# Optimization experiments

Hardware: AMD Instinct MI355X
Metric: run time of the kernel (lower is better)

Reference implementation:

```python
import jax, jax.numpy as jnp
import numpy as np

D_MODEL = 1024
N_HEADS = 16
HEAD_DIM = D_MODEL // N_HEADS


def setup_inputs() -> dict:
    key = jax.random.key(0)
    ks = jax.random.split(key, 5)
    B, S = 4, 2048
    scale = 1.0 / np.sqrt(D_MODEL)
    return {
        "x": jax.random.normal(ks[0], (B, S, D_MODEL), dtype=jnp.float32),
        "W_q": jax.random.normal(ks[1], (D_MODEL, D_MODEL), dtype=jnp.float32) * scale,
        "W_k": jax.random.normal(ks[2], (D_MODEL, D_MODEL), dtype=jnp.float32) * scale,
        "W_v": jax.random.normal(ks[3], (D_MODEL, D_MODEL), dtype=jnp.float32) * scale,
        "W_o": jax.random.normal(ks[4], (D_MODEL, D_MODEL), dtype=jnp.float32) * scale,
    }


def reference(x, W_q, W_k, W_v, W_o):
    B, S, _ = x.shape
    # nn.Linear(d,d,bias=False): y = x @ W.T ; W stored as (out,in)
    def proj(W):
        y = jnp.einsum('bsd,ed->bse', x, W)
        return y.reshape(B, S, N_HEADS, HEAD_DIM).transpose(0, 2, 1, 3)  # (B,H,S,Dh)
    q, k, v = proj(W_q), proj(W_k), proj(W_v)
    scores = jnp.einsum('bhqd,bhkd->bhqk', q, k) / np.sqrt(HEAD_DIM)
    causal = jnp.tril(jnp.ones((S, S), dtype=bool))  # (S,S)
    scores = jnp.where(causal[None, None], scores, -jnp.inf)
    attn = jax.nn.softmax(scores, axis=-1)
    heads = jnp.einsum('bhqk,bhkd->bhqd', attn, v)
    concat = heads.transpose(0, 2, 1, 3).reshape(B, S, D_MODEL)
    return jnp.einsum('bsd,ed->bse', concat, W_o)
```

## Files before the change

### kernel.cpp

```cpp
#include <hip/hip_runtime.h>
#include <hip/hip_bf16.h>

#define D_MODEL 1024
#define N_HEADS 16
#define HEAD_DIM 64
#define BATCH 4
#define SEQ 2048
#define M_ROWS (BATCH * SEQ)

typedef __attribute__((ext_vector_type(8))) __bf16 bf16x8;
typedef __attribute__((ext_vector_type(8))) short short8;
typedef __attribute__((ext_vector_type(4))) float f32x4;

static __device__ __forceinline__ unsigned short f2bf_rne(float f) {
  unsigned int u = __float_as_uint(f);
  u += 0x7FFFu + ((u >> 16) & 1u);
  return (unsigned short)(u >> 16);
}

#if __has_builtin(__builtin_amdgcn_exp2f)
#define EXP2F(x) __builtin_amdgcn_exp2f(x)
#else
#define EXP2F(x) exp2f(x)
#endif

static __device__ __forceinline__ void gl_lds16(const unsigned short* g, unsigned short* l) {
  __builtin_amdgcn_global_load_lds((const __attribute__((address_space(1))) unsigned int*)g,
                                   (__attribute__((address_space(3))) unsigned int*)l, 16, 0, 0);
}

__global__ __launch_bounds__(256) void cvt_all(const float* __restrict__ x,
                                               const float* __restrict__ wq,
                                               const float* __restrict__ wk,
                                               const float* __restrict__ wv,
                                               const float* __restrict__ wo,
                                               unsigned short* __restrict__ xb,
                                               unsigned short* __restrict__ wqb,
                                               unsigned short* __restrict__ wkb,
                                               unsigned short* __restrict__ wvb,
                                               unsigned short* __restrict__ wob) {
  const int bid = blockIdx.x;
  const float* src;
  unsigned short* dst;
  int i;
  if (bid < 8192) {
    src = x; dst = xb; i = bid * 256 + threadIdx.x;
  } else {
    int r = bid - 8192;
    int w = r >> 10;
    i = (r & 1023) * 256 + threadIdx.x;
    switch (w) {
      case 0: src = wq; dst = wqb; break;
      case 1: src = wk; dst = wkb; break;
      case 2: src = wv; dst = wvb; break;
      default: src = wo; dst = wob; break;
    }
  }
  float4 f = reinterpret_cast<const float4*>(src)[i];
  ushort4 o;
  o.x = f2bf_rne(f.x); o.y = f2bf_rne(f.y); o.z = f2bf_rne(f.z); o.w = f2bf_rne(f.w);
  reinterpret_cast<ushort4*>(dst)[i] = o;
}

__global__ __launch_bounds__(256) void qkv_gemm(const unsigned short* __restrict__ A,
                                                const unsigned short* __restrict__ Wq,
                                                const unsigned short* __restrict__ Wk,
                                                const unsigned short* __restrict__ Wv,
                                                unsigned short* __restrict__ Qo,
                                                unsigned short* __restrict__ Ko,
                                                unsigned short* __restrict__ Vt) {
  __shared__ __align__(16) unsigned short smem[16384];
  const int t = threadIdx.x;
  const int widx = blockIdx.x >> 3;
  const int bn = blockIdx.x & 7, bm = blockIdx.y;
  const unsigned short* Bw = (widx == 0) ? Wq : (widx == 1) ? Wk : Wv;
  const float oscale = (widx == 0) ? 0.18033688f : 1.0f;
  const int K = D_MODEL, N = D_MODEL;

  const int wave = t >> 6, lane = t & 63;
  const int wm = (wave >> 1) * 64, wn = (wave & 1) * 64;
  const int lr = lane & 15, quad = lane >> 4;

  const int g0 = wave * 128 + lane, g1 = g0 + 64;
  const int r0 = g0 >> 2, c0 = (g0 & 3) << 3;
  const int r1 = g1 >> 2, c1 = (g1 & 3) << 3;
  const unsigned short* Arow0 = A + (size_t)(bm * 128 + r0) * K + c0;
  const unsigned short* Arow1 = A + (size_t)(bm * 128 + r1) * K + c1;
  const unsigned short* Brow0 = Bw + (size_t)(bn * 128 + r0) * K + c0;
  const unsigned short* Brow1 = Bw + (size_t)(bn * 128 + r1) * K + c1;

  f32x4 acc[4][4] = {};

  gl_lds16(Arow0, &smem[g0 * 8]);
  gl_lds16(Arow1, &smem[g1 * 8]);
  gl_lds16(Brow0, &smem[4096 + g0 * 8]);
  gl_lds16(Brow1, &smem[4096 + g1 * 8]);
  __syncthreads();

  for (int it = 0; it < 32; it++) {
    const int cur = (it & 1) * 8192;
    if (it + 1 < 32) {
      const int nxt = 8192 - cur;
      const int k1 = (it + 1) * 32;
      gl_lds16(Arow0 + k1, &smem[nxt + g0 * 8]);
      gl_lds16(Arow1 + k1, &smem[nxt + g1 * 8]);
      gl_lds16(Brow0 + k1, &smem[nxt + 4096 + g0 * 8]);
      gl_lds16(Brow1 + k1, &smem[nxt + 4096 + g1 * 8]);
    }
    const unsigned short* As = &smem[cur];
    const unsigned short* Bs = &smem[cur + 4096];

    bf16x8 af[4], bfr[4];
#pragma unroll
    for (int mt = 0; mt < 4; mt++)
      af[mt] = __builtin_bit_cast(
          bf16x8, *reinterpret_cast<const short8*>(&As[(wm + mt * 16 + lr) * 32 + quad * 8]));
#pragma unroll
    for (int nt = 0; nt < 4; nt++)
      bfr[nt] = __builtin_bit_cast(
          bf16x8, *reinterpret_cast<const short8*>(&Bs[(wn + nt * 16 + lr) * 32 + quad * 8]));
#pragma unroll
    for (int mt = 0; mt < 4; mt++)
#pragma unroll
      for (int nt = 0; nt < 4; nt++)
        acc[mt][nt] = __builtin_amdgcn_mfma_f32_16x16x32_bf16(af[mt], bfr[nt], acc[mt][nt], 0, 0, 0);
    __syncthreads();
  }

  if (widx < 2) {
    unsigned short* Cp = (widx == 0) ? Qo : Ko;
#pragma unroll
    for (int mt = 0; mt < 4; mt++) {
#pragma unroll
      for (int nt = 0; nt < 4; nt++) {
        int col = bn * 128 + wn + nt * 16 + lr;
#pragma unroll
        for (int r = 0; r < 4; r++) {
          int row = bm * 128 + wm + mt * 16 + quad * 4 + r;
          Cp[(size_t)row * N + col] = f2bf_rne(acc[mt][nt][r] * oscale);
        }
      }
    }
  } else {
    const int b = bm >> 4;
    const int s0 = (bm & 15) * 128;
#pragma unroll
    for (int half = 0; half < 2; half++) {
      __syncthreads();
      if ((wave & 1) == half) {
#pragma unroll
        for (int nt = 0; nt < 4; nt++) {
#pragma unroll
          for (int mt = 0; mt < 4; mt++) {
#pragma unroll
            for (int r = 0; r < 4; r++) {
              int cl = nt * 16 + lr;
              int rl = wm + mt * 16 + quad * 4 + r;
              smem[cl * 136 + rl] = f2bf_rne(acc[mt][nt][r]);
            }
          }
        }
      }
      __syncthreads();
      const int h2 = bn * 2 + half;
      const size_t rowbase = ((size_t)(b * N_HEADS + h2)) * HEAD_DIM;
#pragma unroll
      for (int i = 0; i < 4; i++) {
        int c = i * 256 + t;
        int d = c >> 4, s8 = (c & 15) * 8;
        uint4 v = *reinterpret_cast<const uint4*>(&smem[d * 136 + s8]);
        *reinterpret_cast<uint4*>(Vt + (rowbase + d) * SEQ + s0 + s8) = v;
      }
    }
  }
}

__global__ __launch_bounds__(256) void gemm_bt_f32(const unsigned short* __restrict__ A,
                                                   const unsigned short* __restrict__ Bw,
                                                   float* __restrict__ Cp,
                                                   int M, int N, int K) {
  __shared__ __align__(16) unsigned short smem[12288];
  const int t = threadIdx.x;
  const int bn = blockIdx.x, bm = blockIdx.y;
  const int wave = t >> 6, lane = t & 63;
  const int wm = (wave >> 1) * 64, wn = (wave & 1) * 32;
  const int lr = lane & 15, quad = lane >> 4;

  const int g0 = t, g1 = t + 256;
  const int ar0 = g0 >> 2, ac0 = (g0 & 3) << 3;
  const int ar1 = g1 >> 2, ac1 = (g1 & 3) << 3;
  const int br = t >> 2, bc = (t & 3) << 3;
  const unsigned short* Arow0 = A + (size_t)(bm * 128 + ar0) * K + ac0;
  const unsigned short* Arow1 = A + (size_t)(bm * 128 + ar1) * K + ac1;
  const unsigned short* Brow = Bw + (size_t)(bn * 64 + br) * K + bc;

  f32x4 acc[4][2] = {};

  gl_lds16(Arow0, &smem[g0 * 8]);
  gl_lds16(Arow1, &smem[g1 * 8]);
  gl_lds16(Brow, &smem[4096 + t * 8]);
  __syncthreads();

  const int niter = K / 32;
  for (int it = 0; it < niter; it++) {
    const int cur = (it & 1) * 6144;
    if (it + 1 < niter) {
      const int nxt = 6144 - cur;
      const int k1 = (it + 1) * 32;
      gl_lds16(Arow0 + k1, &smem[nxt + g0 * 8]);
      gl_lds16(Arow1 + k1, &smem[nxt + g1 * 8]);
      gl_lds16(Brow + k1, &smem[nxt + 4096 + t * 8]);
    }
    const unsigned short* As = &smem[cur];
    const unsigned short* Bs = &smem[cur + 4096];

    bf16x8 af[4], bfr[2];
#pragma unroll
    for (int mt = 0; mt < 4; mt++)
      af[mt] = __builtin_bit_cast(
          bf16x8, *reinterpret_cast<const short8*>(&As[(wm + mt * 16 + lr) * 32 + quad * 8]));
#pragma unroll
    for (int nt = 0; nt < 2; nt++)
      bfr[nt] = __builtin_bit_cast(
          bf16x8, *reinterpret_cast<const short8*>(&Bs[(wn + nt * 16 + lr) * 32 + quad * 8]));
#pragma unroll
    for (int mt = 0; mt < 4; mt++)
#pragma unroll
      for (int nt = 0; nt < 2; nt++)
        acc[mt][nt] = __builtin_amdgcn_mfma_f32_16x16x32_bf16(af[mt], bfr[nt], acc[mt][nt], 0, 0, 0);
    __syncthreads();
  }

#pragma unroll
  for (int mt = 0; mt < 4; mt++) {
#pragma unroll
    for (int nt = 0; nt < 2; nt++) {
      int col = bn * 64 + wn + nt * 16 + lr;
#pragma unroll
      for (int r = 0; r < 4; r++) {
        int row = bm * 128 + wm + mt * 16 + quad * 4 + r;
        Cp[(size_t)row * N + col] = acc[mt][nt][r];
      }
    }
  }
}

__global__ __launch_bounds__(512, 2) void attn_causal(const unsigned short* __restrict__ Q,
                                                      const unsigned short* __restrict__ Km,
                                                      const unsigned short* __restrict__ Vt,
                                                      unsigned short* __restrict__ O) {
  __shared__ __align__(16) unsigned short Ks[64 * 72];
  __shared__ __align__(16) unsigned short Vs[64 * 72];
  __shared__ __align__(16) unsigned short Ps[8][32 * 72];

  const int bid = blockIdx.x;
  const int p = bid & 3;
  const int h = (bid >> 2) & 15;
  const int b = bid >> 6;

  const int t = threadIdx.x;
  const int wave = t >> 6, lane = t & 63;
  const int lr = lane & 15, quad = lane >> 4;

  const size_t base = (size_t)b * SEQ * D_MODEL + h * HEAD_DIM;
  const unsigned short* Qb = Q + base;
  const unsigned short* Kb = Km + base;
  const unsigned short* Vb = Vt + (size_t)(b * N_HEADS + h) * HEAD_DIM * SEQ;
  unsigned short* pw = &Ps[wave][0];

  const int sr = t >> 3, sc = (t & 7) << 3;

  for (int ph = 0; ph < 2; ph++) {
    const int qt = ph ? (7 - p) : p;
    const int m0 = qt * 256 + wave * 32;
    const int ntiles = (qt + 1) * 4;

    bf16x8 qf[2][2];
#pragma unroll
    for (int s = 0; s < 2; s++)
#pragma unroll
      for (int kk = 0; kk < 2; kk++)
        qf[s][kk] = __builtin_bit_cast(
            bf16x8, *reinterpret_cast<const short8*>(
                        Qb + (size_t)(m0 + s * 16 + lr) * D_MODEL + kk * 32 + quad * 8));

    f32x4 o_acc[2][4] = {};
    float lsum[2][4] = {};

    uint4 ra = *reinterpret_cast<const uint4*>(Kb + (size_t)sr * D_MODEL + sc);
    uint4 rc = *reinterpret_cast<const uint4*>(Vb + (size_t)sr * SEQ + sc);

    for (int kt = 0; kt < ntiles; kt++) {
      const int kv0 = kt * 64;
      __syncthreads();
      *reinterpret_cast<uint4*>(&Ks[sr * 72 + sc]) = ra;
      *reinterpret_cast<uint4*>(&Vs[sr * 72 + sc]) = rc;
      __syncthreads();
      if (kt + 1 < ntiles) {
        const int kv1 = kv0 + 64;
        ra = *reinterpret_cast<const uint4*>(Kb + (size_t)(kv1 + sr) * D_MODEL + sc);
        rc = *reinterpret_cast<const uint4*>(Vb + (size_t)sr * SEQ + kv1 + sc);
      }

      f32x4 sAcc[2][4] = {};
#pragma unroll
      for (int kk = 0; kk < 2; kk++) {
        bf16x8 kf[4];
#pragma unroll
        for (int j = 0; j < 4; j++)
          kf[j] = __builtin_bit_cast(
              bf16x8, *reinterpret_cast<const short8*>(&Ks[(j * 16 + lr) * 72 + kk * 32 + quad * 8]));
#pragma unroll
        for (int s = 0; s < 2; s++)
#pragma unroll
          for (int j = 0; j < 4; j++)
            sAcc[s][j] =
                __builtin_amdgcn_mfma_f32_16x16x32_bf16(qf[s][kk], kf[j], sAcc[s][j], 0, 0, 0);
      }

      asm volatile("s_waitcnt lgkmcnt(0)" ::: "memory");
#pragma unroll
      for (int s = 0; s < 2; s++) {
        const int msub = m0 + s * 16;
        const bool needmask = (kv0 + 63 > msub);
#pragma unroll
        for (int r = 0; r < 4; r++) {
          const int qpos = msub + quad * 4 + r;
          float e[4];
#pragma unroll
          for (int j = 0; j < 4; j++) e[j] = EXP2F(sAcc[s][j][r]);
          if (needmask) {
#pragma unroll
            for (int j = 0; j < 4; j++)
              if (kv0 + j * 16 + lr > qpos) e[j] = 0.f;
          }
          lsum[s][r] += (e[0] + e[1]) + (e[2] + e[3]);
          unsigned short* pr = &pw[(s * 16 + quad * 4 + r) * 72];
#pragma unroll
          for (int j = 0; j < 4; j++) pr[j * 16 + lr] = f2bf_rne(e[j]);
        }
      }
      asm volatile("s_waitcnt lgkmcnt(0)" ::: "memory");

#pragma unroll
      for (int kk = 0; kk < 2; kk++) {
        bf16x8 pf[2];
#pragma unroll
        for (int s = 0; s < 2; s++)
          pf[s] = __builtin_bit_cast(
              bf16x8,
              *reinterpret_cast<const short8*>(&pw[(s * 16 + lr) * 72 + kk * 32 + quad * 8]));
#pragma unroll
        for (int c = 0; c < 4; c++) {
          bf16x8 vv = __builtin_bit_cast(
              bf16x8, *reinterpret_cast<const short8*>(&Vs[(c * 16 + lr) * 72 + kk * 32 + quad * 8]));
#pragma unroll
          for (int s = 0; s < 2; s++)
            o_acc[s][c] = __builtin_amdgcn_mfma_f32_16x16x32_bf16(pf[s], vv, o_acc[s][c], 0, 0, 0);
        }
      }
    }

#pragma unroll
    for (int s = 0; s < 2; s++) {
#pragma unroll
      for (int r = 0; r < 4; r++) {
        float l = lsum[s][r];
#pragma unroll
        for (int off = 1; off < 16; off <<= 1) l += __shfl_xor(l, off, 64);
        const float inv = 1.f / l;
        const int qpos = m0 + s * 16 + quad * 4 + r;
#pragma unroll
        for (int c = 0; c < 4; c++)
          O[base + (size_t)qpos * D_MODEL + c * 16 + lr] = f2bf_rne(o_acc[s][c][r] * inv);
      }
    }
  }
}

extern "C" void kernel_launch(void* const* d_in, const int* in_sizes, int n_in,
                              void* d_out, int out_size, void* d_ws, size_t ws_size,
                              hipStream_t stream) {
  const float* x  = (const float*)d_in[0];
  const float* Wq = (const float*)d_in[1];
  const float* Wk = (const float*)d_in[2];
  const float* Wv = (const float*)d_in[3];
  const float* Wo = (const float*)d_in[4];
  float* out = (float*)d_out;

  char* ws = (char*)d_ws;
  const size_t SZ_X = (size_t)M_ROWS * D_MODEL * 2;
  const size_t SZ_W = (size_t)D_MODEL * D_MODEL * 2;
  unsigned short* xb  = (unsigned short*)(ws);
  unsigned short* wqb = (unsigned short*)(ws + SZ_X);
  unsigned short* wkb = (unsigned short*)(ws + SZ_X + 1 * SZ_W);
  unsigned short* wvb = (unsigned short*)(ws + SZ_X + 2 * SZ_W);
  unsigned short* wob = (unsigned short*)(ws + SZ_X + 3 * SZ_W);
  unsigned short* Qb  = (unsigned short*)(ws + 1 * SZ_X + 4 * SZ_W);
  unsigned short* Kb  = (unsigned short*)(ws + 2 * SZ_X + 4 * SZ_W);
  unsigned short* Vt  = (unsigned short*)(ws + 3 * SZ_X + 4 * SZ_W);
  unsigned short* Ob  = xb;

  cvt_all<<<12288, 256, 0, stream>>>(x, Wq, Wk, Wv, Wo, xb, wqb, wkb, wvb, wob);

  qkv_gemm<<<dim3(24, 64), 256, 0, stream>>>(xb, wqb, wkb, wvb, Qb, Kb, Vt);

  attn_causal<<<256, 512, 0, stream>>>(Qb, Kb, Vt, Ob);

  gemm_bt_f32<<<dim3(16, 64), 256, 0, stream>>>(Ob, wob, out, M_ROWS, D_MODEL, D_MODEL);
}
```

Before: 269.4 us.

## Use 4 waves with 64 query rows each and double-buffer K/V tiles

```diff
diff --git a/kernel.cpp b/kernel.cpp
--- a/kernel.cpp
+++ b/kernel.cpp
@@ -245,13 +245,12 @@
   }
 }
 
-__global__ __launch_bounds__(512, 2) void attn_causal(const unsigned short* __restrict__ Q,
+__global__ __launch_bounds__(256, 2) void attn_causal(const unsigned short* __restrict__ Q,
                                                       const unsigned short* __restrict__ Km,
                                                       const unsigned short* __restrict__ Vt,
                                                       unsigned short* __restrict__ O) {
-  __shared__ __align__(16) unsigned short Ks[64 * 72];
-  __shared__ __align__(16) unsigned short Vs[64 * 72];
-  __shared__ __align__(16) unsigned short Ps[8][32 * 72];
+  __shared__ __align__(16) unsigned short KV[2][2][64 * 72];
+  __shared__ __align__(16) unsigned short Ps[4][64 * 72];
 
   const int bid = blockIdx.x;
   const int p = bid & 3;
@@ -272,37 +271,57 @@
 
   for (int ph = 0; ph < 2; ph++) {
     const int qt = ph ? (7 - p) : p;
-    const int m0 = qt * 256 + wave * 32;
+    const int m0 = qt * 256 + wave * 64;
     const int ntiles = (qt + 1) * 4;
 
-    bf16x8 qf[2][2];
-#pragma unroll
-    for (int s = 0; s < 2; s++)
+    bf16x8 qf[4][2];
+#pragma unroll
+    for (int s = 0; s < 4; s++)
 #pragma unroll
       for (int kk = 0; kk < 2; kk++)
         qf[s][kk] = __builtin_bit_cast(
             bf16x8, *reinterpret_cast<const short8*>(
                         Qb + (size_t)(m0 + s * 16 + lr) * D_MODEL + kk * 32 + quad * 8));
 
-    f32x4 o_acc[2][4] = {};
-    float lsum[2][4] = {};
+    f32x4 o_acc[4][4] = {};
+    float lsum[4][4] = {};
 
     uint4 ra = *reinterpret_cast<const uint4*>(Kb + (size_t)sr * D_MODEL + sc);
+    uint4 rb = *reinterpret_cast<const uint4*>(Kb + (size_t)(sr + 32) * D_MODEL + sc);
     uint4 rc = *reinterpret_cast<const uint4*>(Vb + (size_t)sr * SEQ + sc);
+    uint4 rd = *reinterpret_cast<const uint4*>(Vb + (size_t)(sr + 32) * SEQ + sc);
+    *reinterpret_cast<uint4*>(&KV[0][0][sr * 72 + sc]) = ra;
+    *reinterpret_cast<uint4*>(&KV[0][0][(sr + 32) * 72 + sc]) = rb;
+    *reinterpret_cast<uint4*>(&KV[0][1][sr * 72 + sc]) = rc;
+    *reinterpret_cast<uint4*>(&KV[0][1][(sr + 32) * 72 + sc]) = rd;
+    if (ntiles > 1) {
+      ra = *reinterpret_cast<const uint4*>(Kb + (size_t)(64 + sr) * D_MODEL + sc);
+      rb = *reinterpret_cast<const uint4*>(Kb + (size_t)(64 + sr + 32) * D_MODEL + sc);
+      rc = *reinterpret_cast<const uint4*>(Vb + (size_t)sr * SEQ + 64 + sc);
+      rd = *reinterpret_cast<const uint4*>(Vb + (size_t)(sr + 32) * SEQ + 64 + sc);
+    }
+    __syncthreads();
 
     for (int kt = 0; kt < ntiles; kt++) {
+      const int cur = kt & 1;
       const int kv0 = kt * 64;
-      __syncthreads();
-      *reinterpret_cast<uint4*>(&Ks[sr * 72 + sc]) = ra;
-      *reinterpret_cast<uint4*>(&Vs[sr * 72 + sc]) = rc;
-      __syncthreads();
       if (kt + 1 < ntiles) {
-        const int kv1 = kv0 + 64;
-        ra = *reinterpret_cast<const uint4*>(Kb + (size_t)(kv1 + sr) * D_MODEL + sc);
-        rc = *reinterpret_cast<const uint4*>(Vb + (size_t)sr * SEQ + kv1 + sc);
-      }
-
-      f32x4 sAcc[2][4] = {};
+        *reinterpret_cast<uint4*>(&KV[1 - cur][0][sr * 72 + sc]) = ra;
+        *reinterpret_cast<uint4*>(&KV[1 - cur][0][(sr + 32) * 72 + sc]) = rb;
+        *reinterpret_cast<uint4*>(&KV[1 - cur][1][sr * 72 + sc]) = rc;
+        *reinterpret_cast<uint4*>(&KV[1 - cur][1][(sr + 32) * 72 + sc]) = rd;
+        if (kt + 2 < ntiles) {
+          const int kv2 = kv0 + 128;
+          ra = *reinterpret_cast<const uint4*>(Kb + (size_t)(kv2 + sr) * D_MODEL + sc);
+          rb = *reinterpret_cast<const uint4*>(Kb + (size_t)(kv2 + sr + 32) * D_MODEL + sc);
+          rc = *reinterpret_cast<const uint4*>(Vb + (size_t)sr * SEQ + kv2 + sc);
+          rd = *reinterpret_cast<const uint4*>(Vb + (size_t)(sr + 32) * SEQ + kv2 + sc);
+        }
+      }
+      const unsigned short* Ks = &KV[cur][0][0];
+      const unsigned short* Vs = &KV[cur][1][0];
+
+      f32x4 sAcc[4][4] = {};
 #pragma unroll
       for (int kk = 0; kk < 2; kk++) {
         bf16x8 kf[4];
@@ -311,7 +330,7 @@
           kf[j] = __builtin_bit_cast(
               bf16x8, *reinterpret_cast<const short8*>(&Ks[(j * 16 + lr) * 72 + kk * 32 + quad * 8]));
 #pragma unroll
-        for (int s = 0; s < 2; s++)
+        for (int s = 0; s < 4; s++)
 #pragma unroll
           for (int j = 0; j < 4; j++)
             sAcc[s][j] =
@@ -320,7 +339,7 @@
 
       asm volatile("s_waitcnt lgkmcnt(0)" ::: "memory");
 #pragma unroll
-      for (int s = 0; s < 2; s++) {
+      for (int s = 0; s < 4; s++) {
         const int msub = m0 + s * 16;
         const bool needmask = (kv0 + 63 > msub);
 #pragma unroll
@@ -344,9 +363,9 @@
 
 #pragma unroll
       for (int kk = 0; kk < 2; kk++) {
-        bf16x8 pf[2];
-#pragma unroll
-        for (int s = 0; s < 2; s++)
+        bf16x8 pf[4];
+#pragma unroll
+        for (int s = 0; s < 4; s++)
           pf[s] = __builtin_bit_cast(
               bf16x8,
               *reinterpret_cast<const short8*>(&pw[(s * 16 + lr) * 72 + kk * 32 + quad * 8]));
@@ -355,14 +374,15 @@
           bf16x8 vv = __builtin_bit_cast(
               bf16x8, *reinterpret_cast<const short8*>(&Vs[(c * 16 + lr) * 72 + kk * 32 + quad * 8]));
 #pragma unroll
-          for (int s = 0; s < 2; s++)
+          for (int s = 0; s < 4; s++)
             o_acc[s][c] = __builtin_amdgcn_mfma_f32_16x16x32_bf16(pf[s], vv, o_acc[s][c], 0, 0, 0);
         }
       }
-    }
-
-#pragma unroll
-    for (int s = 0; s < 2; s++) {
+      __syncthreads();
+    }
+
+#pragma unroll
+    for (int s = 0; s < 4; s++) {
 #pragma unroll
       for (int r = 0; r < 4; r++) {
         float l = lsum[s][r];
@@ -405,7 +425,7 @@
 
   qkv_gemm<<<dim3(24, 64), 256, 0, stream>>>(xb, wqb, wkb, wvb, Qb, Kb, Vt);
 
-  attn_causal<<<256, 512, 0, stream>>>(Qb, Kb, Vt, Ob);
+  attn_causal<<<256, 256, 0, stream>>>(Qb, Kb, Vt, Ob);
 
   gemm_bt_f32<<<dim3(16, 64), 256, 0, stream>>>(Ob, wob, out, M_ROWS, D_MODEL, D_MODEL);
 }
```

Result: slower. 362.3 us (+34.5%).
